# Kernel optimization log

Measured on AMD Instinct MI355X. Metric: run time of the kernel, lower is better.

The kernel has to match this reference:

```python
import jax, jax.numpy as jnp
import numpy as np

G, NODES, H, E = 64, 511, 768, 4096
N = NODES + 1  # +1 graph token


def setup_inputs() -> dict:
    key = jax.random.key(0)
    ks = jax.random.split(key, 7)
    node_emb = jax.random.normal(ks[0], (4, H), dtype=jnp.float32) * 0.02
    node_emb = node_emb.at[0].set(0.0)  # padding_idx=0
    graph_emb = jax.random.normal(ks[1], (1, H), dtype=jnp.float32) * 0.02
    W_l = jax.random.normal(ks[2], (H, H), dtype=jnp.float32) / np.sqrt(H)
    b_l = jnp.zeros((H,), dtype=jnp.float32)
    W_r = jax.random.normal(ks[3], (H, H), dtype=jnp.float32) / np.sqrt(H)
    input_nodes = jax.random.randint(ks[4], (G, NODES), 0, 4, dtype=jnp.int64) if jax.config.jax_enable_x64 else jax.random.randint(ks[4], (G, NODES), 0, 4, dtype=jnp.int32)
    input_edges = jax.random.randint(ks[5], (G, 2, E), 0, N, dtype=jnp.int32)
    return {"input_nodes": input_nodes, "input_edges": input_edges,
            "node_emb": node_emb, "graph_emb": graph_emb,
            "W_l": W_l, "b_l": b_l, "W_r": W_r}


def _sage_conv(x, edges, W_l, b_l, W_r):
    # PyG SAGEConv (mean aggr): out = lin_l(mean_{j in N(i)} x_j) + lin_r(x_i)
    # x: [G, N, H]; edges: [G, 2, E] (row0 = src, row1 = dst)
    g, n, h = x.shape
    src, dst = edges[:, 0, :], edges[:, 1, :]                       # [G, E]
    offs = (jnp.arange(g, dtype=src.dtype) * n)[:, None]
    fs = (src + offs).reshape(-1)                                   # flat src ids
    fd = (dst + offs).reshape(-1)                                   # flat dst ids
    xf = x.reshape(g * n, h)
    msg = xf[fs]                                                    # gather [G*E, H]
    agg = jax.ops.segment_sum(msg, fd, num_segments=g * n)          # scatter-add
    deg = jax.ops.segment_sum(jnp.ones_like(fd, dtype=x.dtype), fd, num_segments=g * n)
    mean = agg / jnp.maximum(deg, 1.0)[:, None]
    out = mean @ W_l.T + b_l + xf @ W_r.T
    return out.reshape(g, n, h)


def reference(input_nodes, input_edges, node_emb, graph_emb, W_l, b_l, W_r):
    g = input_nodes.shape[0]
    node_feature = node_emb[input_nodes]                            # [G, NODES, H]
    graph_token = jnp.broadcast_to(graph_emb[None], (g, 1, node_emb.shape[1]))
    graph_node_feature = jnp.concatenate([graph_token, node_feature], axis=1)  # [G, N, H]
    graph_edge_feature = _sage_conv(graph_node_feature, input_edges, W_l, b_l, W_r)
    return (graph_node_feature, graph_edge_feature)
```

## Files before the change

### kernel.cpp

```cpp
#include <hip/hip_runtime.h>

#define G_   64
#define NODES_ 511
#define NN_  512
#define H_   768
#define E_   4096
#define NTYPE 5

typedef float f32x4 __attribute__((ext_vector_type(4)));

__global__ __launch_bounds__(512)
void prep_kernel(const int* __restrict__ edges,
                 const int* __restrict__ nodes,
                 const float* __restrict__ node_emb,
                 const float* __restrict__ graph_emb,
                 const float* __restrict__ W_l,
                 const float* __restrict__ b_l,
                 const float* __restrict__ W_r,
                 int* __restrict__ cnt,
                 float* __restrict__ P_l,
                 float* __restrict__ P_r)
{
    if (blockIdx.x < G_) {
        __shared__ int hist[NN_ * NTYPE];
        int g = blockIdx.x;
        int t = threadIdx.x;

        #pragma unroll
        for (int i = 0; i < NN_ * NTYPE / 512; ++i)
            hist[t + i * 512] = 0;
        __syncthreads();

        const int* eg = edges + (size_t)g * 2 * E_;
        const int* ng = nodes + (size_t)g * NODES_;
        #pragma unroll
        for (int i = 0; i < E_ / 512; ++i) {
            int e = t + i * 512;
            int src = eg[e];
            int dst = eg[E_ + e];
            int type = (src == 0) ? 0 : (ng[src - 1] + 1);
            atomicAdd(&hist[dst * NTYPE + type], 1);
        }
        __syncthreads();

        int* cg = cnt + (size_t)g * NN_ * NTYPE;
        #pragma unroll
        for (int i = 0; i < NN_ * NTYPE / 512; ++i)
            cg[t + i * 512] = hist[t + i * 512];
    } else {
        int wave = (blockIdx.x - G_) * 8 + (threadIdx.x >> 6);
        int lane = threadIdx.x & 63;
        int m = wave / (NTYPE * H_);
        int r = wave % (NTYPE * H_);
        int t = r / H_;
        int j = r % H_;
        const float* emb = (t == 0) ? graph_emb : (node_emb + (size_t)(t - 1) * H_);
        const float* W   = ((m == 0) ? W_l : W_r) + (size_t)j * H_;

        float a0, a1, a2;
        {
            int k0 = lane * 4;
            f32x4 w0 = *(const f32x4*)(W + k0);
            f32x4 e0 = *(const f32x4*)(emb + k0);
            f32x4 w1 = *(const f32x4*)(W + k0 + 256);
            f32x4 e1 = *(const f32x4*)(emb + k0 + 256);
            f32x4 w2 = *(const f32x4*)(W + k0 + 512);
            f32x4 e2 = *(const f32x4*)(emb + k0 + 512);
            a0 = w0.x * e0.x + w0.y * e0.y + w0.z * e0.z + w0.w * e0.w;
            a1 = w1.x * e1.x + w1.y * e1.y + w1.z * e1.z + w1.w * e1.w;
            a2 = w2.x * e2.x + w2.y * e2.y + w2.z * e2.z + w2.w * e2.w;
        }
        float acc = a0 + a1 + a2;
        #pragma unroll
        for (int off = 32; off; off >>= 1)
            acc += __shfl_xor(acc, off, 64);

        if (lane == 0) {
            if (m == 0) P_l[t * H_ + j] = acc;
            else        P_r[t * H_ + j] = acc + b_l[j];
        }
    }
}

__global__ __launch_bounds__(256)
void out_kernel(const int* __restrict__ nodes,
                const int* __restrict__ cnt,
                const float* __restrict__ node_emb,
                const float* __restrict__ graph_emb,
                const float* __restrict__ P_l,
                const float* __restrict__ P_r,
                float* __restrict__ gnf,
                float* __restrict__ gef)
{
    int tid = blockIdx.x * blockDim.x + threadIdx.x;
    int row = tid / (H_ / 4);
    int j4  = tid % (H_ / 4);
    int g = row >> 9;
    int n = row & (NN_ - 1);

    int type = (n == 0) ? 0 : (nodes[g * NODES_ + n - 1] + 1);

    const int* c = cnt + (size_t)row * NTYPE;
    float c0 = (float)c[0], c1 = (float)c[1], c2 = (float)c[2],
          c3 = (float)c[3], c4 = (float)c[4];
    float deg = c0 + c1 + c2 + c3 + c4;
    float inv = 1.0f / fmaxf(deg, 1.0f);

    int h = j4 * 4;
    f32x4 p0 = *(const f32x4*)(P_l + 0 * H_ + h);
    f32x4 p1 = *(const f32x4*)(P_l + 1 * H_ + h);
    f32x4 p2 = *(const f32x4*)(P_l + 2 * H_ + h);
    f32x4 p3 = *(const f32x4*)(P_l + 3 * H_ + h);
    f32x4 p4 = *(const f32x4*)(P_l + 4 * H_ + h);
    f32x4 pr = *(const f32x4*)(P_r + (size_t)type * H_ + h);

    f32x4 o = (c0 * p0 + c1 * p1 + c2 * p2 + c3 * p3 + c4 * p4) * inv + pr;

    const float* emb = (type == 0) ? graph_emb : (node_emb + (size_t)(type - 1) * H_);
    f32x4 ev = *(const f32x4*)(emb + h);

    size_t off = (size_t)row * H_ + h;
    __builtin_nontemporal_store(ev, (f32x4*)(gnf + off));
    __builtin_nontemporal_store(o,  (f32x4*)(gef + off));
}

extern "C" void kernel_launch(void* const* d_in, const int* in_sizes, int n_in,
                              void* d_out, int out_size, void* d_ws, size_t ws_size,
                              hipStream_t stream)
{
    const int*   input_nodes = (const int*)d_in[0];
    const int*   input_edges = (const int*)d_in[1];
    const float* node_emb    = (const float*)d_in[2];
    const float* graph_emb   = (const float*)d_in[3];
    const float* W_l         = (const float*)d_in[4];
    const float* b_l         = (const float*)d_in[5];
    const float* W_r         = (const float*)d_in[6];

    float* gnf = (float*)d_out;
    float* gef = gnf + (size_t)G_ * NN_ * H_;

    int*   cnt = (int*)d_ws;
    size_t cnt_bytes = (size_t)G_ * NN_ * NTYPE * sizeof(int);
    float* P_l = (float*)((char*)d_ws + cnt_bytes);
    float* P_r = P_l + NTYPE * H_;

    prep_kernel<<<G_ + (2 * NTYPE * H_) / 8, 512, 0, stream>>>(
        input_edges, input_nodes, node_emb, graph_emb, W_l, b_l, W_r,
        cnt, P_l, P_r);

    out_kernel<<<(G_ * NN_ * (H_ / 4)) / 256, 256, 0, stream>>>(
        input_nodes, cnt, node_emb, graph_emb, P_l, P_r, gnf, gef);
}
```

Measured before the change: 225.1 us.

## Fuse edge histogram into output kernel and share W rows across types

```diff
diff --git a/kernel.cpp b/kernel.cpp
--- a/kernel.cpp
+++ b/kernel.cpp
@@ -1,127 +1,155 @@
 #include <hip/hip_runtime.h>
 
-#define G_   64
+#define G_     64
 #define NODES_ 511
-#define NN_  512
-#define H_   768
-#define E_   4096
-#define NTYPE 5
+#define NN_    512
+#define H_     768
+#define E_     4096
+#define NTYPE  5
+#define S_     32
+#define ROWS_  (NN_ / S_)
 
 typedef float f32x4 __attribute__((ext_vector_type(4)));
 
 __global__ __launch_bounds__(512)
-void prep_kernel(const int* __restrict__ edges,
-                 const int* __restrict__ nodes,
-                 const float* __restrict__ node_emb,
+void proj_kernel(const float* __restrict__ node_emb,
                  const float* __restrict__ graph_emb,
                  const float* __restrict__ W_l,
                  const float* __restrict__ b_l,
                  const float* __restrict__ W_r,
-                 int* __restrict__ cnt,
                  float* __restrict__ P_l,
                  float* __restrict__ P_r)
 {
-    if (blockIdx.x < G_) {
-        __shared__ int hist[NN_ * NTYPE];
-        int g = blockIdx.x;
-        int t = threadIdx.x;
+    int wave = blockIdx.x * 8 + (threadIdx.x >> 6);
+    int lane = threadIdx.x & 63;
+    int m = wave / H_;
+    int j = wave % H_;
 
-        #pragma unroll
-        for (int i = 0; i < NN_ * NTYPE / 512; ++i)
-            hist[t + i * 512] = 0;
-        __syncthreads();
+    const float* W = ((m == 0) ? W_l : W_r) + (size_t)j * H_;
+    int k0 = lane * 4;
+    f32x4 w0 = *(const f32x4*)(W + k0);
+    f32x4 w1 = *(const f32x4*)(W + k0 + 256);
+    f32x4 w2 = *(const f32x4*)(W + k0 + 512);
 
-        const int* eg = edges + (size_t)g * 2 * E_;
-        const int* ng = nodes + (size_t)g * NODES_;
-        #pragma unroll
-        for (int i = 0; i < E_ / 512; ++i) {
-            int e = t + i * 512;
-            int src = eg[e];
-            int dst = eg[E_ + e];
-            int type = (src == 0) ? 0 : (ng[src - 1] + 1);
-            atomicAdd(&hist[dst * NTYPE + type], 1);
-        }
-        __syncthreads();
-
-        int* cg = cnt + (size_t)g * NN_ * NTYPE;
-        #pragma unroll
-        for (int i = 0; i < NN_ * NTYPE / 512; ++i)
-            cg[t + i * 512] = hist[t + i * 512];
-    } else {
-        int wave = (blockIdx.x - G_) * 8 + (threadIdx.x >> 6);
-        int lane = threadIdx.x & 63;
-        int m = wave / (NTYPE * H_);
-        int r = wave % (NTYPE * H_);
-        int t = r / H_;
-        int j = r % H_;
+    float acc[NTYPE];
+    #pragma unroll
+    for (int t = 0; t < NTYPE; ++t) {
         const float* emb = (t == 0) ? graph_emb : (node_emb + (size_t)(t - 1) * H_);
-        const float* W   = ((m == 0) ? W_l : W_r) + (size_t)j * H_;
-
-        float a0, a1, a2;
-        {
-            int k0 = lane * 4;
-            f32x4 w0 = *(const f32x4*)(W + k0);
-            f32x4 e0 = *(const f32x4*)(emb + k0);
-            f32x4 w1 = *(const f32x4*)(W + k0 + 256);
-            f32x4 e1 = *(const f32x4*)(emb + k0 + 256);
-            f32x4 w2 = *(const f32x4*)(W + k0 + 512);
-            f32x4 e2 = *(const f32x4*)(emb + k0 + 512);
-            a0 = w0.x * e0.x + w0.y * e0.y + w0.z * e0.z + w0.w * e0.w;
-            a1 = w1.x * e1.x + w1.y * e1.y + w1.z * e1.z + w1.w * e1.w;
-            a2 = w2.x * e2.x + w2.y * e2.y + w2.z * e2.z + w2.w * e2.w;
-        }
-        float acc = a0 + a1 + a2;
+        f32x4 e0 = *(const f32x4*)(emb + k0);
+        f32x4 e1 = *(const f32x4*)(emb + k0 + 256);
+        f32x4 e2 = *(const f32x4*)(emb + k0 + 512);
+        acc[t] = w0.x*e0.x + w0.y*e0.y + w0.z*e0.z + w0.w*e0.w
+               + w1.x*e1.x + w1.y*e1.y + w1.z*e1.z + w1.w*e1.w
+               + w2.x*e2.x + w2.y*e2.y + w2.z*e2.z + w2.w*e2.w;
+    }
+    #pragma unroll
+    for (int t = 0; t < NTYPE; ++t) {
         #pragma unroll
         for (int off = 32; off; off >>= 1)
-            acc += __shfl_xor(acc, off, 64);
+            acc[t] += __shfl_xor(acc[t], off, 64);
+    }
 
-        if (lane == 0) {
-            if (m == 0) P_l[t * H_ + j] = acc;
-            else        P_r[t * H_ + j] = acc + b_l[j];
+    if (lane == 0) {
+        if (m == 0) {
+            #pragma unroll
+            for (int t = 0; t < NTYPE; ++t) P_l[t * H_ + j] = acc[t];
+        } else {
+            float b = b_l[j];
+            #pragma unroll
+            for (int t = 0; t < NTYPE; ++t) P_r[t * H_ + j] = acc[t] + b;
         }
     }
 }
 
 __global__ __launch_bounds__(256)
-void out_kernel(const int* __restrict__ nodes,
-                const int* __restrict__ cnt,
-                const float* __restrict__ node_emb,
-                const float* __restrict__ graph_emb,
-                const float* __restrict__ P_l,
-                const float* __restrict__ P_r,
-                float* __restrict__ gnf,
-                float* __restrict__ gef)
+void fused_kernel(const int* __restrict__ nodes,
+                  const int* __restrict__ edges,
+                  const float* __restrict__ node_emb,
+                  const float* __restrict__ graph_emb,
+                  const float* __restrict__ P_l,
+                  const float* __restrict__ P_r,
+                  float* __restrict__ gnf,
+                  float* __restrict__ gef)
 {
-    int tid = blockIdx.x * blockDim.x + threadIdx.x;
-    int row = tid / (H_ / 4);
-    int j4  = tid % (H_ / 4);
-    int g = row >> 9;
-    int n = row & (NN_ - 1);
+    int g  = blockIdx.x >> 5;
+    int s  = blockIdx.x & (S_ - 1);
+    int lo = s * ROWS_;
+    int t  = threadIdx.x;
 
-    int type = (n == 0) ? 0 : (nodes[g * NODES_ + n - 1] + 1);
+    __shared__ int   hist[ROWS_ * NTYPE];
+    __shared__ float a_s[ROWS_][NTYPE];
+    __shared__ int   type_s[ROWS_];
 
-    const int* c = cnt + (size_t)row * NTYPE;
-    float c0 = (float)c[0], c1 = (float)c[1], c2 = (float)c[2],
-          c3 = (float)c[3], c4 = (float)c[4];
-    float deg = c0 + c1 + c2 + c3 + c4;
-    float inv = 1.0f / fmaxf(deg, 1.0f);
+    if (t < ROWS_ * NTYPE) hist[t] = 0;
+    __syncthreads();
 
-    int h = j4 * 4;
-    f32x4 p0 = *(const f32x4*)(P_l + 0 * H_ + h);
-    f32x4 p1 = *(const f32x4*)(P_l + 1 * H_ + h);
-    f32x4 p2 = *(const f32x4*)(P_l + 2 * H_ + h);
-    f32x4 p3 = *(const f32x4*)(P_l + 3 * H_ + h);
-    f32x4 p4 = *(const f32x4*)(P_l + 4 * H_ + h);
-    f32x4 pr = *(const f32x4*)(P_r + (size_t)type * H_ + h);
+    const int* eg = edges + (size_t)g * 2 * E_;
+    const int* ng = nodes + (size_t)g * NODES_;
 
-    f32x4 o = (c0 * p0 + c1 * p1 + c2 * p2 + c3 * p3 + c4 * p4) * inv + pr;
+    #pragma unroll
+    for (int i = 0; i < E_ / 256; ++i) {
+        int e   = t + i * 256;
+        int dst = eg[E_ + e];
+        unsigned d = (unsigned)(dst - lo);
+        if (d < ROWS_) {
+            int src  = eg[e];
+            int type = (src == 0) ? 0 : (ng[src - 1] + 1);
+            atomicAdd(&hist[d * NTYPE + type], 1);
+        }
+    }
+    __syncthreads();
 
-    const float* emb = (type == 0) ? graph_emb : (node_emb + (size_t)(type - 1) * H_);
-    f32x4 ev = *(const f32x4*)(emb + h);
+    if (t < ROWS_) {
+        float c0 = (float)hist[t * NTYPE + 0];
+        float c1 = (float)hist[t * NTYPE + 1];
+        float c2 = (float)hist[t * NTYPE + 2];
+        float c3 = (float)hist[t * NTYPE + 3];
+        float c4 = (float)hist[t * NTYPE + 4];
+        float inv = 1.0f / fmaxf(c0 + c1 + c2 + c3 + c4, 1.0f);
+        a_s[t][0] = c0 * inv;
+        a_s[t][1] = c1 * inv;
+        a_s[t][2] = c2 * inv;
+        a_s[t][3] = c3 * inv;
+        a_s[t][4] = c4 * inv;
+        int n = lo + t;
+        type_s[t] = (n == 0) ? 0 : (ng[n - 1] + 1);
+    }
+    __syncthreads();
 
-    size_t off = (size_t)row * H_ + h;
-    __builtin_nontemporal_store(ev, (f32x4*)(gnf + off));
-    __builtin_nontemporal_store(o,  (f32x4*)(gef + off));
+    int w    = t >> 6;
+    int lane = t & 63;
+    int k0   = lane * 4;
+
+    f32x4 pl[NTYPE][3];
+    #pragma unroll
+    for (int tt = 0; tt < NTYPE; ++tt) {
+        #pragma unroll
+        for (int c = 0; c < 3; ++c)
+            pl[tt][c] = *(const f32x4*)(P_l + (size_t)tt * H_ + k0 + c * 256);
+    }
+
+    size_t base = ((size_t)g * NN_ + lo) * H_;
+
+    #pragma unroll
+    for (int rr = 0; rr < ROWS_ / 4; ++rr) {
+        int r  = rr * 4 + w;
+        int ty = type_s[r];
+        float a0 = a_s[r][0], a1 = a_s[r][1], a2 = a_s[r][2],
+              a3 = a_s[r][3], a4 = a_s[r][4];
+        const float* prr = P_r + (size_t)ty * H_;
+        const float* er  = (ty == 0) ? graph_emb : (node_emb + (size_t)(ty - 1) * H_);
+        size_t roff = base + (size_t)r * H_ + k0;
+
+        #pragma unroll
+        for (int c = 0; c < 3; ++c) {
+            f32x4 pr = *(const f32x4*)(prr + k0 + c * 256);
+            f32x4 ev = *(const f32x4*)(er  + k0 + c * 256);
+            f32x4 o  = a0 * pl[0][c] + a1 * pl[1][c] + a2 * pl[2][c]
+                     + a3 * pl[3][c] + a4 * pl[4][c] + pr;
+            *(f32x4*)(gnf + roff + c * 256) = ev;
+            *(f32x4*)(gef + roff + c * 256) = o;
+        }
+    }
 }
 
 extern "C" void kernel_launch(void* const* d_in, const int* in_sizes, int n_in,
@@ -139,15 +167,12 @@
     float* gnf = (float*)d_out;
     float* gef = gnf + (size_t)G_ * NN_ * H_;
 
-    int*   cnt = (int*)d_ws;
-    size_t cnt_bytes = (size_t)G_ * NN_ * NTYPE * sizeof(int);
-    float* P_l = (float*)((char*)d_ws + cnt_bytes);
+    float* P_l = (float*)d_ws;
     float* P_r = P_l + NTYPE * H_;
 
-    prep_kernel<<<G_ + (2 * NTYPE * H_) / 8, 512, 0, stream>>>(
-        input_edges, input_nodes, node_emb, graph_emb, W_l, b_l, W_r,
-        cnt, P_l, P_r);
+    proj_kernel<<<(2 * H_) / 8, 512, 0, stream>>>(
+        node_emb, graph_emb, W_l, b_l, W_r, P_l, P_r);
 
-    out_kernel<<<(G_ * NN_ * (H_ / 4)) / 256, 256, 0, stream>>>(
-        input_nodes, cnt, node_emb, graph_emb, P_l, P_r, gnf, gef);
+    fused_kernel<<<G_ * S_, 256, 0, stream>>>(
+        input_nodes, input_edges, node_emb, graph_emb, P_l, P_r, gnf, gef);
 }
```

New measurement: 241.6 us. 7.3% more time.
